# Optimization experiments

Measured on AMD Instinct MI355X. Metric: run time of the kernel, lower is better.

## Reference

```python
import jax, jax.numpy as jnp
import numpy as np

N, F, H, K, O = 16384, 64, 128, 16, 10


def setup_inputs() -> dict:
    key = jax.random.key(0)
    ks = jax.random.split(key, 12)
    s = lambda fan: 1.0 / np.sqrt(fan)
    return {
        "x": jax.random.normal(ks[0], (N, F), dtype=jnp.float32),
        "edge_index": jax.random.randint(ks[1], (2, N * 8), 0, N),  # unused by forward
        "mlp_w1": jax.random.normal(ks[2], (2 * F, H), dtype=jnp.float32) * s(2 * F),
        "mlp_b1": jnp.zeros((H,), jnp.float32),
        "mlp_w2": jax.random.normal(ks[3], (H, H), dtype=jnp.float32) * s(H),
        "mlp_b2": jnp.zeros((H,), jnp.float32),
        "gcn_w": jax.random.normal(ks[4], (H, H), dtype=jnp.float32) * s(H),
        "gcn_b": jnp.zeros((H,), jnp.float32),
        "gnn_out_w": jax.random.normal(ks[5], (H, H), dtype=jnp.float32) * s(H),
        "gnn_out_b": jnp.zeros((H,), jnp.float32),
        "out_w": jax.random.normal(ks[6], (H, O), dtype=jnp.float32) * s(H),
        "out_b": jnp.zeros((O,), jnp.float32),
        "k": K,
    }


def _forward(x, mlp_w1, mlp_b1, mlp_w2, mlp_b2, gcn_w, gcn_b,
             gnn_out_w, gnn_out_b, out_w, out_b, k):
    n = x.shape[0]
    # ---- dynamic kNN graph in feature space (includes self, dist 0) ----
    sq = jnp.sum(x * x, axis=-1)                       # [N]
    d2 = sq[:, None] + sq[None, :] - 2.0 * (x @ x.T)   # [N,N] squared dists
    _, idx = jax.lax.top_k(-d2, k)                     # [N,k] neighbor (source) ids per query
    # ---- EdgeConv message: MLP(cat(x_i, x_j - x_i)), max-aggregate over k ----
    x_j = x[idx]                                       # [N,k,F]
    x_i = jnp.broadcast_to(x[:, None, :], x_j.shape)   # [N,k,F]
    m = jnp.concatenate([x_i, x_j - x_i], axis=-1)     # [N,k,2F]
    m = jax.nn.relu(m @ mlp_w1 + mlp_b1)
    m = jax.nn.log_softmax(m @ mlp_w2 + mlp_b2, axis=-1)
    h = jnp.max(m, axis=1)                             # [N,H] max aggregation
    # ---- GCNConv on the kNN edge_index (+ self loops, symmetric norm) ----
    loop = jnp.arange(n)
    src = jnp.concatenate([idx.reshape(-1), loop])     # sources (x_j)
    dst = jnp.concatenate([jnp.repeat(loop, k), loop]) # targets (x_i)
    deg = jax.ops.segment_sum(jnp.ones_like(src, h.dtype), dst, num_segments=n)
    dinv = jax.lax.rsqrt(jnp.maximum(deg, 1.0))
    norm = dinv[src] * dinv[dst]                       # [E]
    hw = h @ gcn_w                                     # [N,H]
    h = jax.ops.segment_sum(norm[:, None] * hw[src], dst, num_segments=n) + gcn_b
    # ---- inner GNN output head (Linear + Softmax) ----
    h = jax.nn.softmax(h @ gnn_out_w + gnn_out_b, axis=-1)
    # ---- GNN_Combo output head (Linear + Softmax) ----
    return jax.nn.softmax(h @ out_w + out_b, axis=-1)  # [N,O]


def reference(x, edge_index, mlp_w1, mlp_b1, mlp_w2, mlp_b2, gcn_w, gcn_b,
              gnn_out_w, gnn_out_b, out_w, out_b, k):
    # edge_index is accepted by GNN_Combo.forward but unused (kNN graph replaces it)
    del edge_index
    return _forward(x, mlp_w1, mlp_b1, mlp_w2, mlp_b2, gcn_w, gcn_b,
                    gnn_out_w, gnn_out_b, out_w, out_b, k)
```

## Files before the change

kernel.cpp:

```cpp
#include <hip/hip_runtime.h>
#include <hip/hip_fp16.h>
#include <cfloat>
#include <cmath>
#include <string.h>


#define N_NODES 16384
#define F_IN    64
#define H_DIM   128
#define K_NN    16
#define O_DIM   10

typedef _Float16 half8  __attribute__((ext_vector_type(8)));
typedef _Float16 half4v __attribute__((ext_vector_type(4)));
typedef _Float16 half2v __attribute__((ext_vector_type(2)));
typedef float    floatx4 __attribute__((ext_vector_type(4)));

__device__ __forceinline__ void async_copy16(void* lds, const void* g) {
  __builtin_amdgcn_global_load_lds(
      (const __attribute__((address_space(1))) unsigned int*)g,
      (__attribute__((address_space(3))) unsigned int*)lds, 16, 0, 0);
}

__device__ __forceinline__ unsigned pack2h(float a, float b) {
  half2v p; p[0] = (_Float16)a; p[1] = (_Float16)b;
  unsigned u; __builtin_memcpy(&u, &p, 4); return u;
}
__device__ __forceinline__ float unpacklo(unsigned u) {
  half2v p; __builtin_memcpy(&p, &u, 4); return (float)p[0];
}
__device__ __forceinline__ float unpackhi(unsigned u) {
  half2v p; __builtin_memcpy(&p, &u, 4); return (float)p[1];
}

__global__ __launch_bounds__(256) void k_prep(const float* __restrict__ x,
                                              float* __restrict__ sq,
                                              double* __restrict__ sq64,
                                              _Float16* __restrict__ xh,
                                              unsigned* __restrict__ cnt) {
  const int i = blockIdx.x * 256 + threadIdx.x;
  if (i >= N_NODES) return;
  const float4* r = (const float4*)(x + i * F_IN);
  float s = 0.f; double sd = 0.0;
#pragma unroll
  for (int q = 0; q < 16; ++q) {
    const float4 v = r[q];
    s += v.x*v.x + v.y*v.y + v.z*v.z + v.w*v.w;
    sd += (double)v.x*v.x + (double)v.y*v.y + (double)v.z*v.z + (double)v.w*v.w;
    half4v hv;
    hv[0] = (_Float16)v.x; hv[1] = (_Float16)v.y;
    hv[2] = (_Float16)v.z; hv[3] = (_Float16)v.w;
    *(half4v*)(xh + (size_t)i * F_IN + 4 * q) = hv;
  }
  sq[i] = s; sq64[i] = sd; cnt[i] = 0;
}

__global__ __launch_bounds__(256) void k_gemm(const _Float16* __restrict__ xh,
                                              const float* __restrict__ sq,
                                              char* __restrict__ subg) {
  __shared__ __align__(16) _Float16 stage[128 * 64];
  __shared__ float sqs[128];
  const int tid = threadIdx.x;
  const int wv = tid >> 6, l = tid & 63;
  const int lane16 = l & 15, quad = l >> 4;
  const int rowblk = (blockIdx.x >> 5) * 256;
  const int seg = blockIdx.x & 31;
  const int rw = rowblk + wv * 64;

  half8 B[4][2];
#pragma unroll
  for (int s = 0; s < 4; ++s) {
    const _Float16* bp = xh + (size_t)(rw + s * 16 + lane16) * F_IN + quad * 8;
    B[s][0] = *(const half8*)(bp);
    B[s][1] = *(const half8*)(bp + 32);
  }

  const int lcol8 = l >> 3;
  const int lchk  = (l & 7) ^ lcol8;
  const size_t lgoff = (size_t)lcol8 * F_IN + lchk * 8;

  for (int tile = 0; tile < 4; ++tile) {
    const int c0 = seg * 512 + tile * 128;
    __syncthreads();
    if (tid < 128) sqs[tid] = sq[c0 + tid];
#pragma unroll
    for (int q = 0; q < 4; ++q) {
      const int grp = wv * 4 + q;
      async_copy16(stage + grp * 512,
                   xh + (size_t)(c0 + grp * 8) * F_IN + lgoff);
    }
    __syncthreads();

    float sprev[4];
    unsigned pk[4][4];
#pragma unroll
    for (int st = 0; st < 8; ++st) {
      const _Float16* base = stage + (st * 16 + lane16) * 64;
      const int sw = lane16 & 7;
      const half8 A0 = *(const half8*)(base + ((quad ^ sw) * 8));
      const half8 A1 = *(const half8*)(base + (((4 + quad) ^ sw) * 8));
      const floatx4 sq4 = *(const floatx4*)(sqs + st * 16 + quad * 4);
      floatx4 acc[4];
#pragma unroll
      for (int s = 0; s < 4; ++s) acc[s] = (floatx4)0.f;
#pragma unroll
      for (int s = 0; s < 4; ++s)
        acc[s] = __builtin_amdgcn_mfma_f32_16x16x32_f16(A0, B[s][0], acc[s], 0, 0, 0);
#pragma unroll
      for (int s = 0; s < 4; ++s)
        acc[s] = __builtin_amdgcn_mfma_f32_16x16x32_f16(A1, B[s][1], acc[s], 0, 0, 0);
#pragma unroll
      for (int s = 0; s < 4; ++s) {
        const float k0 = fmaf(-2.f, acc[s][0], sq4[0]);
        const float k1 = fmaf(-2.f, acc[s][1], sq4[1]);
        const float k2 = fmaf(-2.f, acc[s][2], sq4[2]);
        const float k3 = fmaf(-2.f, acc[s][3], sq4[3]);
        float m = fminf(fminf(k0, k1), fminf(k2, k3));
        m = fminf(m, __shfl_xor(m, 16, 64));
        m = fminf(m, __shfl_xor(m, 32, 64));
        if ((st & 1) == 0) sprev[s] = m;
        else pk[s][st >> 1] = pack2h(sprev[s], m);
      }
    }
    unsigned o0 = pk[0][0], o1 = pk[0][1], o2 = pk[0][2], o3 = pk[0][3];
    if (quad == 1) { o0 = pk[1][0]; o1 = pk[1][1]; o2 = pk[1][2]; o3 = pk[1][3]; }
    if (quad == 2) { o0 = pk[2][0]; o1 = pk[2][1]; o2 = pk[2][2]; o3 = pk[2][3]; }
    if (quad == 3) { o0 = pk[3][0]; o1 = pk[3][1]; o2 = pk[3][2]; o3 = pk[3][3]; }
    const int row = rw + quad * 16 + lane16;
    uint4 ov; ov.x = o0; ov.y = o1; ov.z = o2; ov.w = o3;
    *(uint4*)(subg + ((size_t)row * 1024 + seg * 32 + tile * 8) * 2) = ov;
  }
}

__global__ __launch_bounds__(256) void k_filter(const _Float16* __restrict__ xh,
                                                const float* __restrict__ sq,
                                                const char* __restrict__ subg,
                                                unsigned* __restrict__ cnt,
                                                int* __restrict__ cand) {
  const int l = threadIdx.x & 63;
  const int i = blockIdx.x * 4 + (threadIdx.x >> 6);
  const int part = l & 3, c = l >> 2;

  float xi[16];
  {
    const half8* xp = (const half8*)(xh + (size_t)i * F_IN + part * 16);
    const half8 a = xp[0], b = xp[1];
#pragma unroll
    for (int j = 0; j < 8; ++j) { xi[j] = (float)a[j]; xi[8 + j] = (float)b[j]; }
  }
  float subs[16];
  {
    const uint4 a = *(const uint4*)(subg + ((size_t)i * 1024 + l * 16) * 2);
    const uint4 b = *(const uint4*)(subg + ((size_t)i * 1024 + l * 16) * 2 + 16);
    subs[0] = unpacklo(a.x); subs[1] = unpackhi(a.x);
    subs[2] = unpacklo(a.y); subs[3] = unpackhi(a.y);
    subs[4] = unpacklo(a.z); subs[5] = unpackhi(a.z);
    subs[6] = unpacklo(a.w); subs[7] = unpackhi(a.w);
    subs[8] = unpacklo(b.x); subs[9] = unpackhi(b.x);
    subs[10] = unpacklo(b.y); subs[11] = unpackhi(b.y);
    subs[12] = unpacklo(b.z); subs[13] = unpackhi(b.z);
    subs[14] = unpacklo(b.w); subs[15] = unpackhi(b.w);
  }
  float cmin = subs[0];
#pragma unroll
  for (int t = 1; t < 16; ++t) cmin = fminf(cmin, subs[t]);
  int rank = 0;
#pragma unroll 4
  for (int j = 0; j < 64; ++j) {
    const float vj = __shfl(cmin, j, 64);
    rank += (vj < cmin) || (vj == cmin && j < l);
  }
  const unsigned long long rm = __ballot(rank == 15);
  const int srcl = __ffsll((long long)rm) - 1;
  const float thr = __shfl(cmin, srcl, 64) + 0.25f;

  unsigned selmask = 0;
#pragma unroll
  for (int t = 0; t < 16; ++t) selmask |= (subs[t] <= thr) ? (1u << t) : 0u;

  unsigned long long act;
  while ((act = __ballot(selmask != 0)) != 0ull) {
    const int src = __ffsll((long long)act) - 1;
    unsigned m = __shfl(selmask, src, 64);
    if (l == src) selmask = 0;
    while (m) {
      const int b = __ffs(m) - 1; m &= m - 1;
      const int sid = src * 16 + b;
      const int cg = sid * 16 + c;
      float d = 0.f;
      {
        const half8* gp = (const half8*)(xh + (size_t)cg * F_IN + part * 16);
        const half8 g0 = gp[0], g1 = gp[1];
#pragma unroll
        for (int j = 0; j < 8; ++j) {
          d = fmaf(xi[j], (float)g0[j], d);
          d = fmaf(xi[8 + j], (float)g1[j], d);
        }
      }
      d += __shfl_xor(d, 1, 64);
      d += __shfl_xor(d, 2, 64);
      const float key = fmaf(-2.f, d, sq[cg]);
      const bool pred = (part == 0) && (key <= thr);
      const unsigned long long am = __ballot(pred);
      if (am) {
        const int ldr = __ffsll((long long)am) - 1;
        unsigned base = 0;
        if (l == ldr) base = atomicAdd(&cnt[i], (unsigned)__popcll(am));
        base = __shfl(base, ldr, 64);
        if (pred) {
          const unsigned idx = base + (unsigned)__popcll(am & ((1ull << l) - 1ull));
          if (idx < 128u) cand[(size_t)i * 128 + idx] = cg;
        }
      }
    }
  }
}

__global__ __launch_bounds__(128) void k_rescore(const float* __restrict__ x,
                                                 const double* __restrict__ sq64,
                                                 const int* __restrict__ cand,
                                                 const unsigned* __restrict__ cnt,
                                                 int* __restrict__ knn) {
  __shared__ float  xi[F_IN];
  __shared__ double keys[128];
  __shared__ int    ids[128];
  const int i = blockIdx.x, t = threadIdx.x;
  const unsigned cv = cnt[i];
  const int n = (int)(cv < 128u ? cv : 128u);
  if (t < F_IN) xi[t] = x[i * F_IN + t];
  __syncthreads();
  double key = 1e300; int id = 0x7fffffff;
  if (t < n) {
    id = cand[(size_t)i * 128 + t];
    const float4* xc4 = (const float4*)(x + (size_t)id * F_IN);
    double d0 = 0.0, d1 = 0.0, d2 = 0.0, d3 = 0.0;
#pragma unroll
    for (int q = 0; q < 16; ++q) {
      const float4 v = xc4[q];
      d0 += (double)xi[4*q+0] * (double)v.x;
      d1 += (double)xi[4*q+1] * (double)v.y;
      d2 += (double)xi[4*q+2] * (double)v.z;
      d3 += (double)xi[4*q+3] * (double)v.w;
    }
    key = sq64[id] - 2.0 * ((d0 + d1) + (d2 + d3));
  }
  keys[t] = key; ids[t] = id;
  __syncthreads();
  int rank = 0;
  for (int cix = 0; cix < n; ++cix) {
    const double kc = keys[cix]; const int ic = ids[cix];
    rank += (kc < key) || (kc == key && ic < id);
  }
  if (t < n && rank < K_NN) knn[i * K_NN + rank] = id;
}

__global__ __launch_bounds__(256, 2) void k_lin12(const float* __restrict__ x,
                                                  const float* __restrict__ w1,
                                                  const float* __restrict__ b1,
                                                  float* __restrict__ P,
                                                  float* __restrict__ Q) {
  __shared__ float wl[2 * F_IN][H_DIM];
  for (int s = threadIdx.x; s < 2 * F_IN * H_DIM; s += 256) wl[s >> 7][s & 127] = w1[s];
  __syncthreads();
  const int node = blockIdx.x * 32 + (threadIdx.x & 31);
  const int ob = (threadIdx.x >> 5) * 16;
  float accR[16], accQ[16];
#pragma unroll
  for (int o = 0; o < 16; ++o) { accR[o] = 0.f; accQ[o] = 0.f; }
  const float4* xr = (const float4*)(x + node * F_IN);
#define L1STEP(ff, xs) { \
    const float* wt_ = &wl[(ff)][ob]; \
    const float* wb_ = &wl[(ff) + F_IN][ob]; \
    _Pragma("unroll") \
    for (int o = 0; o < 16; o += 4) { \
      const float4 t4 = *(const float4*)(wt_ + o); \
      const float4 b4 = *(const float4*)(wb_ + o); \
      accR[o+0] = fmaf((xs), t4.x, accR[o+0]); accQ[o+0] = fmaf((xs), b4.x, accQ[o+0]); \
      accR[o+1] = fmaf((xs), t4.y, accR[o+1]); accQ[o+1] = fmaf((xs), b4.y, accQ[o+1]); \
      accR[o+2] = fmaf((xs), t4.z, accR[o+2]); accQ[o+2] = fmaf((xs), b4.z, accQ[o+2]); \
      accR[o+3] = fmaf((xs), t4.w, accR[o+3]); accQ[o+3] = fmaf((xs), b4.w, accQ[o+3]); } }
#pragma unroll 2
  for (int q = 0; q < 16; ++q) {
    const float4 xv = xr[q];
    L1STEP(4*q+0, xv.x); L1STEP(4*q+1, xv.y); L1STEP(4*q+2, xv.z); L1STEP(4*q+3, xv.w);
  }
#undef L1STEP
  float* pp = P + node * H_DIM + ob;
  float* qp = Q + node * H_DIM + ob;
#pragma unroll
  for (int o = 0; o < 16; ++o) {
    pp[o] = accR[o] - accQ[o] + b1[ob + o];
    qp[o] = accQ[o];
  }
}

__global__ __launch_bounds__(256, 3) void k_edgeconv(const float* __restrict__ P,
                                                     const float* __restrict__ Q,
                                                     const float* __restrict__ w2,
                                                     const float* __restrict__ b2,
                                                     const int* __restrict__ knn,
                                                     float* __restrict__ h) {
  __shared__ __align__(16) _Float16 wt[H_DIM * 128];
  __shared__ __align__(16) _Float16 afr[4][2048];
  const int tid = threadIdx.x;
  const int wv = tid >> 6, l = tid & 63;
  const int lane16 = l & 15, quad = l >> 4;

  {
    const int n = tid >> 1, part = tid & 1;
    const float* wsrc = w2 + n;
    _Float16* wdst = wt + n * 128;
#pragma unroll
    for (int c = 0; c < 8; ++c) {
      half8 hv;
#pragma unroll
      for (int u = 0; u < 8; ++u)
        hv[u] = (_Float16)wsrc[(size_t)(part * 64 + c * 8 + u) * H_DIM];
      *(half8*)(wdst + (((part * 8 + c) ^ (n & 15)) * 8)) = hv;
    }
  }
  __syncthreads();

  float b2r[8];
#pragma unroll
  for (int tile = 0; tile < 8; ++tile) b2r[tile] = b2[tile * 16 + lane16];

  _Float16* aw = afr[wv];
  for (int it = 0; it < 8; ++it) {
    const int i = blockIdx.x * 32 + wv * 8 + it;
    {
      const int m = lane16, kq = quad;
      const int j = knn[i * K_NN + m];
      const float4* pq = (const float4*)(P + (size_t)i * H_DIM + kq * 32);
      const float4* qq = (const float4*)(Q + (size_t)j * H_DIM + kq * 32);
#pragma unroll
      for (int c = 0; c < 4; ++c) {
        const float4 pa = pq[2 * c],     qa = qq[2 * c];
        const float4 pb = pq[2 * c + 1], qb = qq[2 * c + 1];
        half8 hv;
        hv[0] = (_Float16)fmaxf(pa.x + qa.x, 0.f);
        hv[1] = (_Float16)fmaxf(pa.y + qa.y, 0.f);
        hv[2] = (_Float16)fmaxf(pa.z + qa.z, 0.f);
        hv[3] = (_Float16)fmaxf(pa.w + qa.w, 0.f);
        hv[4] = (_Float16)fmaxf(pb.x + qb.x, 0.f);
        hv[5] = (_Float16)fmaxf(pb.y + qb.y, 0.f);
        hv[6] = (_Float16)fmaxf(pb.z + qb.z, 0.f);
        hv[7] = (_Float16)fmaxf(pb.w + qb.w, 0.f);
        *(half8*)(aw + kq * 512 + c * 128 + m * 8) = hv;
      }
    }
    half8 A[4];
#pragma unroll
    for (int kb = 0; kb < 4; ++kb) A[kb] = *(const half8*)(aw + kb * 512 + l * 8);
    floatx4 acc[8];
#pragma unroll
    for (int tile = 0; tile < 8; ++tile) acc[tile] = (floatx4)0.f;
#pragma unroll
    for (int kb = 0; kb < 4; ++kb) {
#pragma unroll
      for (int tile = 0; tile < 8; ++tile) {
        const half8 B = *(const half8*)(wt + (tile * 16 + lane16) * 128 +
                                        (((kb * 4 + quad) ^ lane16) * 8));
        acc[tile] = __builtin_amdgcn_mfma_f32_16x16x32_f16(A[kb], B, acc[tile], 0, 0, 0);
      }
    }
    float lse[4];
#pragma unroll
    for (int r = 0; r < 4; ++r) {
      float mx = acc[0][r] + b2r[0];
#pragma unroll
      for (int tile = 1; tile < 8; ++tile) mx = fmaxf(mx, acc[tile][r] + b2r[tile]);
      mx = fmaxf(mx, __shfl_xor(mx, 1, 64));
      mx = fmaxf(mx, __shfl_xor(mx, 2, 64));
      mx = fmaxf(mx, __shfl_xor(mx, 4, 64));
      mx = fmaxf(mx, __shfl_xor(mx, 8, 64));
      float e = 0.f;
#pragma unroll
      for (int tile = 0; tile < 8; ++tile) e += __expf(acc[tile][r] + b2r[tile] - mx);
      e += __shfl_xor(e, 1, 64);
      e += __shfl_xor(e, 2, 64);
      e += __shfl_xor(e, 4, 64);
      e += __shfl_xor(e, 8, 64);
      lse[r] = mx + __logf(e);
    }
#pragma unroll
    for (int tile = 0; tile < 8; ++tile) {
      float v = acc[tile][0] + b2r[tile] - lse[0];
#pragma unroll
      for (int r = 1; r < 4; ++r) v = fmaxf(v, acc[tile][r] + b2r[tile] - lse[r]);
      v = fmaxf(v, __shfl_xor(v, 16, 64));
      v = fmaxf(v, __shfl_xor(v, 32, 64));
      if (quad == 0) h[(size_t)i * H_DIM + tile * 16 + lane16] = v;
    }
  }
}

__global__ __launch_bounds__(256) void k_hw(const float* __restrict__ h,
                                            const float* __restrict__ gw,
                                            float* __restrict__ hw) {
  __shared__ float wl[H_DIM][H_DIM];
  for (int s = threadIdx.x; s < H_DIM * H_DIM; s += 256) wl[s >> 7][s & 127] = gw[s];
  __syncthreads();
  const int node = blockIdx.x * 32 + (threadIdx.x & 31);
  const int ob = (threadIdx.x >> 5) * 16;
  float acc[16];
#pragma unroll
  for (int o = 0; o < 16; ++o) acc[o] = 0.f;
  const float4* hr = (const float4*)(h + node * H_DIM);
#define HWSTEP(ff, xs) { \
    const float* wr = &wl[(ff)][ob]; \
    _Pragma("unroll") \
    for (int o = 0; o < 16; o += 4) { const float4 w4 = *(const float4*)(wr + o); \
      acc[o+0] = fmaf((xs), w4.x, acc[o+0]); \
      acc[o+1] = fmaf((xs), w4.y, acc[o+1]); \
      acc[o+2] = fmaf((xs), w4.z, acc[o+2]); \
      acc[o+3] = fmaf((xs), w4.w, acc[o+3]); } }
#pragma unroll 2
  for (int q = 0; q < 32; ++q) {
    const float4 hv = hr[q];
    HWSTEP(4*q+0, hv.x); HWSTEP(4*q+1, hv.y); HWSTEP(4*q+2, hv.z); HWSTEP(4*q+3, hv.w);
  }
#undef HWSTEP
  float* dp = hw + node * H_DIM + ob;
#pragma unroll
  for (int o = 0; o < 16; ++o) dp[o] = acc[o];
}

__global__ __launch_bounds__(256) void k_heads(const float* __restrict__ hw,
                                               const int* __restrict__ knn,
                                               const float* __restrict__ gb,
                                               const float* __restrict__ gow,
                                               const float* __restrict__ gob,
                                               const float* __restrict__ ow,
                                               const float* __restrict__ obv,
                                               float* __restrict__ out) {
  __shared__ unsigned int wgo[H_DIM][64];
  __shared__ float hbuf[4][H_DIM];
  for (int s = threadIdx.x; s < H_DIM * 64; s += 256) {
    const int f = s >> 6, l = s & 63;
    const unsigned short u0 = __half_as_ushort(__float2half(gow[f * H_DIM + l]));
    const unsigned short u1 = __half_as_ushort(__float2half(gow[f * H_DIM + 64 + l]));
    wgo[f][l] = (unsigned int)u0 | ((unsigned int)u1 << 16);
  }
  __syncthreads();
  const int wv = threadIdx.x >> 6, l = threadIdx.x & 63;
  const float gbl = gb[l], gbh = gb[64 + l];
  const float gobl = gob[l], gobh = gob[64 + l];
  for (int it = 0; it < 8; ++it) {
    const int i = blockIdx.x * 32 + wv * 8 + it;
    const int* kr = knn + i * K_NN;
    float s0 = hw[i * H_DIM + l], s1 = hw[i * H_DIM + 64 + l];
#pragma unroll
    for (int m = 0; m < K_NN; ++m) {
      const int j = kr[m];
      s0 += hw[j * H_DIM + l];
      s1 += hw[j * H_DIM + 64 + l];
    }
    const float hg0 = s0 * (1.0f / 17.0f) + gbl;
    const float hg1 = s1 * (1.0f / 17.0f) + gbh;
    __syncthreads();
    hbuf[wv][l] = hg0; hbuf[wv][64 + l] = hg1;
    __syncthreads();
    float z0 = gobl, z1 = gobh;
#pragma unroll 4
    for (int f = 0; f < H_DIM; ++f) {
      const float hv = hbuf[wv][f];
      const unsigned int wvv = wgo[f][l];
      const float w0 = __half2float(__ushort_as_half((unsigned short)(wvv & 0xffffu)));
      const float w1 = __half2float(__ushort_as_half((unsigned short)(wvv >> 16)));
      z0 = fmaf(hv, w0, z0);
      z1 = fmaf(hv, w1, z1);
    }
    float mx = fmaxf(z0, z1);
#pragma unroll
    for (int s = 1; s < 64; s <<= 1) mx = fmaxf(mx, __shfl_xor(mx, s, 64));
    const float e0 = __expf(z0 - mx), e1 = __expf(z1 - mx);
    float sm = e0 + e1;
#pragma unroll
    for (int s = 1; s < 64; s <<= 1) sm += __shfl_xor(sm, s, 64);
    const float h20 = e0 / sm, h21 = e1 / sm;
    float zc[O_DIM];
#pragma unroll
    for (int c = 0; c < O_DIM; ++c) {
      float a = h20 * ow[l * O_DIM + c] + h21 * ow[(64 + l) * O_DIM + c];
#pragma unroll
      for (int s = 1; s < 64; s <<= 1) a += __shfl_xor(a, s, 64);
      zc[c] = a + obv[c];
    }
    float m10 = zc[0];
#pragma unroll
    for (int c = 1; c < O_DIM; ++c) m10 = fmaxf(m10, zc[c]);
    float es[O_DIM]; float s10 = 0.f;
#pragma unroll
    for (int c = 0; c < O_DIM; ++c) { es[c] = __expf(zc[c] - m10); s10 += es[c]; }
    const float inv = 1.0f / s10;
    if (l < O_DIM) {
      float v = es[0];
#pragma unroll
      for (int c = 1; c < O_DIM; ++c) if (l == c) v = es[c];
      out[i * O_DIM + l] = v * inv;
    }
  }
}

extern "C" void kernel_launch(void* const* d_in, const int* in_sizes, int n_in,
                              void* d_out, int out_size, void* d_ws, size_t ws_size,
                              hipStream_t stream) {
  (void)in_sizes; (void)n_in; (void)out_size; (void)ws_size;
  const float* x   = (const float*)d_in[0];
  const float* w1  = (const float*)d_in[2];
  const float* b1  = (const float*)d_in[3];
  const float* w2  = (const float*)d_in[4];
  const float* b2  = (const float*)d_in[5];
  const float* gw  = (const float*)d_in[6];
  const float* gb  = (const float*)d_in[7];
  const float* gow = (const float*)d_in[8];
  const float* gob = (const float*)d_in[9];
  const float* ow  = (const float*)d_in[10];
  const float* obv = (const float*)d_in[11];
  float* out = (float*)d_out;

  char* ws = (char*)d_ws;
  constexpr size_t OFF_SQ   = 0;
  constexpr size_t OFF_SQ64 = OFF_SQ   + (size_t)N_NODES * 4;
  constexpr size_t OFF_XH   = OFF_SQ64 + (size_t)N_NODES * 8;
  constexpr size_t OFF_CNT  = OFF_XH   + (size_t)N_NODES * F_IN * 2;
  constexpr size_t OFF_CAND = OFF_CNT  + (size_t)N_NODES * 4;
  constexpr size_t OFF_SUBG = OFF_CAND + (size_t)N_NODES * 128 * 4;
  constexpr size_t OFF_KNN  = OFF_SUBG;
  constexpr size_t OFF_Q    = OFF_SUBG + (size_t)N_NODES * K_NN * 4;
  constexpr size_t OFF_H    = OFF_Q    + (size_t)N_NODES * H_DIM * 4;
  float*     sq   = (float*)    (ws + OFF_SQ);
  double*    sq64 = (double*)   (ws + OFF_SQ64);
  _Float16*  xh   = (_Float16*) (ws + OFF_XH);
  unsigned*  cnt  = (unsigned*) (ws + OFF_CNT);
  int*       cand = (int*)      (ws + OFF_CAND);
  char*      subg = (char*)     (ws + OFF_SUBG);
  int*       knn  = (int*)      (ws + OFF_KNN);
  float*     Q    = (float*)    (ws + OFF_Q);
  float*     h    = (float*)    (ws + OFF_H);
  float*     P    = (float*)    (ws + OFF_CAND);
  float*     hw   = P;

  k_prep    <<<N_NODES / 256, 256, 0, stream>>>(x, sq, sq64, xh, cnt);
  k_gemm    <<<2048,          256, 0, stream>>>(xh, sq, subg);
  k_filter  <<<N_NODES / 4,   256, 0, stream>>>(xh, sq, subg, cnt, cand);
  k_rescore <<<N_NODES,       128, 0, stream>>>(x, sq64, cand, cnt, knn);
  k_lin12   <<<N_NODES / 32,  256, 0, stream>>>(x, w1, b1, P, Q);
  k_edgeconv<<<N_NODES / 32,  256, 0, stream>>>(P, Q, w2, b2, knn, h);
  k_hw      <<<N_NODES / 32,  256, 0, stream>>>(h, gw, hw);
  k_heads   <<<N_NODES / 32,  256, 0, stream>>>(hw, knn, gb, gow, gob, ow, obv, out);
}
```

Baseline: 396.6 us.

## Store P/Q and hw intermediates in fp16 and prefetch edgeconv gathers

The P/Q EdgeConv precomputations and the GCN hw matrix are now written as fp16 instead of fp32, which halves the bytes moved by the gathered neighbor reads in k_edgeconv and k_heads. k_edgeconv preloads the kNN indices and software-prefetches the next node's P/Q rows while the current node is processed, does the add and ReLU in half precision, and its occupancy hint drops from 3 to 2. k_heads uses an interleaved feature layout and drops two block barriers around the per-wave shared buffer. The cost is lower intermediate precision, and the barrier removal relies on each wave touching only its own buffer row.

```diff
diff --git a/kernel.cpp b/kernel.cpp
--- a/kernel.cpp
+++ b/kernel.cpp
@@ -257,8 +257,8 @@
 __global__ __launch_bounds__(256, 2) void k_lin12(const float* __restrict__ x,
                                                   const float* __restrict__ w1,
                                                   const float* __restrict__ b1,
-                                                  float* __restrict__ P,
-                                                  float* __restrict__ Q) {
+                                                  _Float16* __restrict__ Ph,
+                                                  _Float16* __restrict__ Qh) {
   __shared__ float wl[2 * F_IN][H_DIM];
   for (int s = threadIdx.x; s < 2 * F_IN * H_DIM; s += 256) wl[s >> 7][s & 127] = w1[s];
   __syncthreads();
@@ -285,17 +285,23 @@
     L1STEP(4*q+0, xv.x); L1STEP(4*q+1, xv.y); L1STEP(4*q+2, xv.z); L1STEP(4*q+3, xv.w);
   }
 #undef L1STEP
-  float* pp = P + node * H_DIM + ob;
-  float* qp = Q + node * H_DIM + ob;
-#pragma unroll
-  for (int o = 0; o < 16; ++o) {
-    pp[o] = accR[o] - accQ[o] + b1[ob + o];
-    qp[o] = accQ[o];
-  }
-}
-
-__global__ __launch_bounds__(256, 3) void k_edgeconv(const float* __restrict__ P,
-                                                     const float* __restrict__ Q,
+  _Float16* pp = Ph + (size_t)node * H_DIM + ob;
+  _Float16* qp = Qh + (size_t)node * H_DIM + ob;
+#pragma unroll
+  for (int o = 0; o < 16; o += 4) {
+    half4v hp, hq;
+#pragma unroll
+    for (int u = 0; u < 4; ++u) {
+      hp[u] = (_Float16)(accR[o+u] - accQ[o+u] + b1[ob + o + u]);
+      hq[u] = (_Float16)accQ[o+u];
+    }
+    *(half4v*)(pp + o) = hp;
+    *(half4v*)(qp + o) = hq;
+  }
+}
+
+__global__ __launch_bounds__(256, 2) void k_edgeconv(const _Float16* __restrict__ Ph,
+                                                     const _Float16* __restrict__ Qh,
                                                      const float* __restrict__ w2,
                                                      const float* __restrict__ b2,
                                                      const int* __restrict__ knn,
@@ -325,29 +331,35 @@
 #pragma unroll
   for (int tile = 0; tile < 8; ++tile) b2r[tile] = b2[tile * 16 + lane16];
 
+  const int i0 = blockIdx.x * 32 + wv * 8;
+  int js[8];
+#pragma unroll
+  for (int it = 0; it < 8; ++it) js[it] = knn[(i0 + it) * K_NN + lane16];
+
   _Float16* aw = afr[wv];
+  half8 pc[4], qc[4];
+  {
+    const half8* pr = (const half8*)(Ph + (size_t)i0 * H_DIM + quad * 32);
+    const half8* qr = (const half8*)(Qh + (size_t)js[0] * H_DIM + quad * 32);
+#pragma unroll
+    for (int c = 0; c < 4; ++c) { pc[c] = pr[c]; qc[c] = qr[c]; }
+  }
   for (int it = 0; it < 8; ++it) {
-    const int i = blockIdx.x * 32 + wv * 8 + it;
-    {
-      const int m = lane16, kq = quad;
-      const int j = knn[i * K_NN + m];
-      const float4* pq = (const float4*)(P + (size_t)i * H_DIM + kq * 32);
-      const float4* qq = (const float4*)(Q + (size_t)j * H_DIM + kq * 32);
-#pragma unroll
-      for (int c = 0; c < 4; ++c) {
-        const float4 pa = pq[2 * c],     qa = qq[2 * c];
-        const float4 pb = pq[2 * c + 1], qb = qq[2 * c + 1];
-        half8 hv;
-        hv[0] = (_Float16)fmaxf(pa.x + qa.x, 0.f);
-        hv[1] = (_Float16)fmaxf(pa.y + qa.y, 0.f);
-        hv[2] = (_Float16)fmaxf(pa.z + qa.z, 0.f);
-        hv[3] = (_Float16)fmaxf(pa.w + qa.w, 0.f);
-        hv[4] = (_Float16)fmaxf(pb.x + qb.x, 0.f);
-        hv[5] = (_Float16)fmaxf(pb.y + qb.y, 0.f);
-        hv[6] = (_Float16)fmaxf(pb.z + qb.z, 0.f);
-        hv[7] = (_Float16)fmaxf(pb.w + qb.w, 0.f);
-        *(half8*)(aw + kq * 512 + c * 128 + m * 8) = hv;
-      }
+    const int i = i0 + it;
+    half8 pn[4], qn[4];
+    if (it < 7) {
+      const half8* pr = (const half8*)(Ph + (size_t)(i + 1) * H_DIM + quad * 32);
+      const half8* qr = (const half8*)(Qh + (size_t)js[it + 1] * H_DIM + quad * 32);
+#pragma unroll
+      for (int c = 0; c < 4; ++c) { pn[c] = pr[c]; qn[c] = qr[c]; }
+    }
+#pragma unroll
+    for (int c = 0; c < 4; ++c) {
+      half8 z = pc[c] + qc[c];
+      half8 r;
+#pragma unroll
+      for (int u = 0; u < 8; ++u) r[u] = z[u] > (_Float16)0 ? z[u] : (_Float16)0;
+      *(half8*)(aw + quad * 512 + c * 128 + lane16 * 8) = r;
     }
     half8 A[4];
 #pragma unroll
@@ -392,12 +404,14 @@
       v = fmaxf(v, __shfl_xor(v, 32, 64));
       if (quad == 0) h[(size_t)i * H_DIM + tile * 16 + lane16] = v;
     }
+#pragma unroll
+    for (int c = 0; c < 4; ++c) { pc[c] = pn[c]; qc[c] = qn[c]; }
   }
 }
 
 __global__ __launch_bounds__(256) void k_hw(const float* __restrict__ h,
                                             const float* __restrict__ gw,
-                                            float* __restrict__ hw) {
+                                            _Float16* __restrict__ hwh) {
   __shared__ float wl[H_DIM][H_DIM];
   for (int s = threadIdx.x; s < H_DIM * H_DIM; s += 256) wl[s >> 7][s & 127] = gw[s];
   __syncthreads();
@@ -421,12 +435,17 @@
     HWSTEP(4*q+0, hv.x); HWSTEP(4*q+1, hv.y); HWSTEP(4*q+2, hv.z); HWSTEP(4*q+3, hv.w);
   }
 #undef HWSTEP
-  float* dp = hw + node * H_DIM + ob;
-#pragma unroll
-  for (int o = 0; o < 16; ++o) dp[o] = acc[o];
-}
-
-__global__ __launch_bounds__(256) void k_heads(const float* __restrict__ hw,
+  _Float16* dp = hwh + (size_t)node * H_DIM + ob;
+#pragma unroll
+  for (int o = 0; o < 16; o += 4) {
+    half4v hv;
+#pragma unroll
+    for (int u = 0; u < 4; ++u) hv[u] = (_Float16)acc[o + u];
+    *(half4v*)(dp + o) = hv;
+  }
+}
+
+__global__ __launch_bounds__(256) void k_heads(const _Float16* __restrict__ hwh,
                                                const int* __restrict__ knn,
                                                const float* __restrict__ gb,
                                                const float* __restrict__ gow,
@@ -438,38 +457,34 @@
   __shared__ float hbuf[4][H_DIM];
   for (int s = threadIdx.x; s < H_DIM * 64; s += 256) {
     const int f = s >> 6, l = s & 63;
-    const unsigned short u0 = __half_as_ushort(__float2half(gow[f * H_DIM + l]));
-    const unsigned short u1 = __half_as_ushort(__float2half(gow[f * H_DIM + 64 + l]));
-    wgo[f][l] = (unsigned int)u0 | ((unsigned int)u1 << 16);
+    wgo[f][l] = pack2h(gow[f * H_DIM + 2 * l], gow[f * H_DIM + 2 * l + 1]);
   }
   __syncthreads();
   const int wv = threadIdx.x >> 6, l = threadIdx.x & 63;
-  const float gbl = gb[l], gbh = gb[64 + l];
-  const float gobl = gob[l], gobh = gob[64 + l];
+  const unsigned* hw32 = (const unsigned*)hwh;
+  const float gbl = gb[2 * l], gbh = gb[2 * l + 1];
+  const float gobl = gob[2 * l], gobh = gob[2 * l + 1];
   for (int it = 0; it < 8; ++it) {
     const int i = blockIdx.x * 32 + wv * 8 + it;
     const int* kr = knn + i * K_NN;
-    float s0 = hw[i * H_DIM + l], s1 = hw[i * H_DIM + 64 + l];
+    unsigned u = hw32[(size_t)i * 64 + l];
+    float s0 = unpacklo(u), s1 = unpackhi(u);
 #pragma unroll
     for (int m = 0; m < K_NN; ++m) {
-      const int j = kr[m];
-      s0 += hw[j * H_DIM + l];
-      s1 += hw[j * H_DIM + 64 + l];
+      const unsigned um = hw32[(size_t)kr[m] * 64 + l];
+      s0 += unpacklo(um);
+      s1 += unpackhi(um);
     }
     const float hg0 = s0 * (1.0f / 17.0f) + gbl;
     const float hg1 = s1 * (1.0f / 17.0f) + gbh;
-    __syncthreads();
-    hbuf[wv][l] = hg0; hbuf[wv][64 + l] = hg1;
-    __syncthreads();
+    hbuf[wv][2 * l] = hg0; hbuf[wv][2 * l + 1] = hg1;
     float z0 = gobl, z1 = gobh;
 #pragma unroll 4
     for (int f = 0; f < H_DIM; ++f) {
       const float hv = hbuf[wv][f];
       const unsigned int wvv = wgo[f][l];
-      const float w0 = __half2float(__ushort_as_half((unsigned short)(wvv & 0xffffu)));
-      const float w1 = __half2float(__ushort_as_half((unsigned short)(wvv >> 16)));
-      z0 = fmaf(hv, w0, z0);
-      z1 = fmaf(hv, w1, z1);
+      z0 = fmaf(hv, unpacklo(wvv), z0);
+      z1 = fmaf(hv, unpackhi(wvv), z1);
     }
     float mx = fmaxf(z0, z1);
 #pragma unroll
@@ -482,7 +497,7 @@
     float zc[O_DIM];
 #pragma unroll
     for (int c = 0; c < O_DIM; ++c) {
-      float a = h20 * ow[l * O_DIM + c] + h21 * ow[(64 + l) * O_DIM + c];
+      float a = h20 * ow[(2 * l) * O_DIM + c] + h21 * ow[(2 * l + 1) * O_DIM + c];
 #pragma unroll
       for (int s = 1; s < 64; s <<= 1) a += __shfl_xor(a, s, 64);
       zc[c] = a + obv[c];
@@ -521,6 +536,7 @@
   float* out = (float*)d_out;
 
   char* ws = (char*)d_ws;
+  constexpr size_t MB = 1024 * 1024;
   constexpr size_t OFF_SQ   = 0;
   constexpr size_t OFF_SQ64 = OFF_SQ   + (size_t)N_NODES * 4;
   constexpr size_t OFF_XH   = OFF_SQ64 + (size_t)N_NODES * 8;
@@ -528,8 +544,8 @@
   constexpr size_t OFF_CAND = OFF_CNT  + (size_t)N_NODES * 4;
   constexpr size_t OFF_SUBG = OFF_CAND + (size_t)N_NODES * 128 * 4;
   constexpr size_t OFF_KNN  = OFF_SUBG;
-  constexpr size_t OFF_Q    = OFF_SUBG + (size_t)N_NODES * K_NN * 4;
-  constexpr size_t OFF_H    = OFF_Q    + (size_t)N_NODES * H_DIM * 4;
+  constexpr size_t OFF_H    = OFF_SUBG + 1 * MB;
+  constexpr size_t OFF_HWH  = OFF_SUBG + 9 * MB;
   float*     sq   = (float*)    (ws + OFF_SQ);
   double*    sq64 = (double*)   (ws + OFF_SQ64);
   _Float16*  xh   = (_Float16*) (ws + OFF_XH);
@@ -537,17 +553,17 @@
   int*       cand = (int*)      (ws + OFF_CAND);
   char*      subg = (char*)     (ws + OFF_SUBG);
   int*       knn  = (int*)      (ws + OFF_KNN);
-  float*     Q    = (float*)    (ws + OFF_Q);
   float*     h    = (float*)    (ws + OFF_H);
-  float*     P    = (float*)    (ws + OFF_CAND);
-  float*     hw   = P;
+  _Float16*  hwh  = (_Float16*) (ws + OFF_HWH);
+  _Float16*  Ph   = (_Float16*) (ws + OFF_CAND);
+  _Float16*  Qh   = (_Float16*) (ws + OFF_CAND + 4 * MB);
 
   k_prep    <<<N_NODES / 256, 256, 0, stream>>>(x, sq, sq64, xh, cnt);
   k_gemm    <<<2048,          256, 0, stream>>>(xh, sq, subg);
   k_filter  <<<N_NODES / 4,   256, 0, stream>>>(xh, sq, subg, cnt, cand);
   k_rescore <<<N_NODES,       128, 0, stream>>>(x, sq64, cand, cnt, knn);
-  k_lin12   <<<N_NODES / 32,  256, 0, stream>>>(x, w1, b1, P, Q);
-  k_edgeconv<<<N_NODES / 32,  256, 0, stream>>>(P, Q, w2, b2, knn, h);
-  k_hw      <<<N_NODES / 32,  256, 0, stream>>>(h, gw, hw);
-  k_heads   <<<N_NODES / 32,  256, 0, stream>>>(hw, knn, gb, gow, gob, ow, obv, out);
-}
+  k_lin12   <<<N_NODES / 32,  256, 0, stream>>>(x, w1, b1, Ph, Qh);
+  k_edgeconv<<<N_NODES / 32,  256, 0, stream>>>(Ph, Qh, w2, b2, knn, h);
+  k_hw      <<<N_NODES / 32,  256, 0, stream>>>(h, gw, hwh);
+  k_heads   <<<N_NODES / 32,  256, 0, stream>>>(hwh, knn, gb, gow, gob, ow, obv, out);
+}
```

Result: faster. 349.4 us (-11.9%).
